# Kernel tuning notes

Hardware: AMD Instinct MI355X
Metric: run time of the kernel (lower is better)

The kernel has to match this reference:

```python
import jax, jax.numpy as jnp
import numpy as np
import math

D_MODEL = 768
N_HEADS = 12
HEAD_DIM = D_MODEL // N_HEADS
B, T = 2, 4096


def setup_inputs() -> dict:
    key = jax.random.key(0)
    k1, k2, k3, k4 = jax.random.split(key, 4)
    x = jax.random.normal(k1, (B, T, D_MODEL), dtype=jnp.float32)
    mask = jax.random.randint(k2, (B, T), 0, 2).astype(jnp.bool_)
    # torch Linear init scale ~ 1/sqrt(fan_in); use scaled normal for stability
    w_qkv = jax.random.normal(k3, (3 * D_MODEL, D_MODEL), dtype=jnp.float32) / math.sqrt(D_MODEL)
    w_proj = jax.random.normal(k4, (D_MODEL, D_MODEL), dtype=jnp.float32) / math.sqrt(D_MODEL)
    b_proj = jnp.zeros((D_MODEL,), dtype=jnp.float32)
    return {"x": x, "mask": mask, "w_qkv": w_qkv, "w_proj": w_proj, "b_proj": b_proj}


def reference(x, mask, w_qkv, w_proj, b_proj):
    Bb, Tt, D = x.shape
    H, Hd = N_HEADS, HEAD_DIM
    scale = math.sqrt(Hd)
    # qkv projection (bias-free): (B,T,3D) -> (3,B,H,T,Hd)
    qkv = jnp.einsum('btd,ed->bte', x, w_qkv)
    qkv = qkv.reshape(Bb, Tt, 3, H, Hd).transpose(2, 0, 3, 1, 4)
    q, k, v = qkv[0], qkv[1], qkv[2]
    # full T x T scores (faithful to non-fused original)
    attn = jnp.einsum('bhqd,bhkd->bhqk', q, k) / scale
    attn = jnp.where(mask[:, None, None, :], -jnp.inf, attn)
    attn = jax.nn.softmax(attn, axis=-1)  # dropout p=0 -> identity
    out = jnp.einsum('bhqk,bhkd->bhqd', attn, v)
    out = out.transpose(0, 2, 1, 3).reshape(Bb, Tt, D)
    return jnp.einsum('btd,ed->bte', out, w_proj) + b_proj
```

## Files before the change

kernel.cpp:

```cpp
#include <hip/hip_runtime.h>

#define D_MODEL 768
#define N_HEADS 12
#define SEQ 4096
#define KVB 64

typedef __attribute__((ext_vector_type(4))) float f32x4;
typedef __attribute__((ext_vector_type(16))) float f32x16;
typedef __attribute__((ext_vector_type(8))) short bf16x8;
typedef __attribute__((ext_vector_type(4))) unsigned short u16x4;

typedef __attribute__((address_space(3))) void lds_void;
typedef __attribute__((address_space(1))) const void glb_void;

static __device__ __forceinline__ void gld_lds16(const void* g, void* l) {
    __builtin_amdgcn_global_load_lds((glb_void*)g, (lds_void*)l, 16, 0, 0);
}

static __device__ __forceinline__ unsigned short f32_bf16(float f) {
    union { float f; unsigned int u; } c; c.f = f;
    unsigned int u = c.u;
    u += 0x7FFFu + ((u >> 16) & 1u);
    return (unsigned short)(u >> 16);
}

static __device__ __forceinline__ unsigned int cvtpk(float lo, float hi) {
    unsigned int r;
    asm("v_cvt_pk_bf16_f32 %0, %1, %2" : "=v"(r) : "v"(lo), "v"(hi));
    return r;
}

__global__ void cvt_bf16(const float* __restrict__ in, unsigned short* __restrict__ out, int n) {
    int i = (blockIdx.x * blockDim.x + threadIdx.x) * 4;
    int stride = gridDim.x * blockDim.x * 4;
    for (; i < n; i += stride) {
        f32x4 v = *(const f32x4*)(in + i);
        u16x4 o;
        o[0] = f32_bf16(v[0]); o[1] = f32_bf16(v[1]);
        o[2] = f32_bf16(v[2]); o[3] = f32_bf16(v[3]);
        *(u16x4*)(out + i) = o;
    }
}

#define QSCL 0.18033688f

__global__ __launch_bounds__(256) void qkv_gemm(const unsigned short* __restrict__ A,
                                                const unsigned short* __restrict__ Bw,
                                                unsigned short* __restrict__ qb,
                                                unsigned short* __restrict__ kb,
                                                unsigned short* __restrict__ vb) {
    __shared__ __attribute__((aligned(16))) unsigned short lA[128*32];
    __shared__ __attribute__((aligned(16))) unsigned short lB[128*32];
    const int K = 768;
    int tid = threadIdx.x;
    int wave = tid >> 6, lane = tid & 63;
    int qr = (wave >> 1) * 64, qc = (wave & 1) * 64;
    int m0 = blockIdx.x * 128, n0 = blockIdx.y * 128;
    f32x4 acc[4][4] = {};
    const int sl = (((lane >> 4) ^ (lane & 3)) * 16);

    for (int kt = 0; kt < K; kt += 32) {
        __syncthreads();
        #pragma unroll
        for (int i = 0; i < 2; ++i) {
            int c = i*256 + tid;
            int row = c >> 2;
            int col = ((c & 3) ^ (row & 3)) * 8;
            char* dA = (char*)lA + (i*256 + wave*64)*16;
            char* dB = (char*)lB + (i*256 + wave*64)*16;
            gld_lds16(A  + (size_t)(m0 + row) * K + kt + col, dA);
            gld_lds16(Bw + (size_t)(n0 + row) * K + kt + col, dB);
        }
        __syncthreads();
        bf16x8 af[4], bfr[4];
        #pragma unroll
        for (int m = 0; m < 4; ++m)
            af[m] = *(bf16x8*)((char*)lA + (qr + m*16 + (lane & 15))*64 + sl);
        #pragma unroll
        for (int n = 0; n < 4; ++n)
            bfr[n] = *(bf16x8*)((char*)lB + (qc + n*16 + (lane & 15))*64 + sl);
        #pragma unroll
        for (int m = 0; m < 4; ++m)
            #pragma unroll
            for (int n = 0; n < 4; ++n)
                acc[m][n] = __builtin_amdgcn_mfma_f32_16x16x32_bf16(af[m], bfr[n], acc[m][n], 0, 0, 0);
    }
    #pragma unroll
    for (int n = 0; n < 4; ++n) {
        int colg = n0 + qc + n*16 + (lane & 15);
        int s = colg / 768;
        int rem = colg - s * 768;
        int h = rem >> 6, d = rem & 63;
        if (s == 2) {
            #pragma unroll
            for (int m = 0; m < 4; ++m) {
                int rowb = m0 + qr + m*16 + (lane >> 4)*4;
                int bb = rowb >> 12, t0 = rowb & 4095;
                int t0p = (t0 & ~12) | ((t0 & 4) << 1) | ((t0 & 8) >> 1);
                u16x4 pk;
                #pragma unroll
                for (int r = 0; r < 4; ++r) pk[r] = f32_bf16(acc[m][n][r]);
                *(u16x4*)(vb + ((size_t)((bb*12 + h)*64 + d))*4096 + t0p) = pk;
            }
        } else {
            unsigned short* dst = (s == 0) ? qb : kb;
            float scl = (s == 0) ? QSCL : 1.0f;
            #pragma unroll
            for (int m = 0; m < 4; ++m) {
                int rowb = m0 + qr + m*16 + (lane >> 4)*4;
                #pragma unroll
                for (int r = 0; r < 4; ++r) {
                    int row = rowb + r;
                    int bb = row >> 12, t = row & 4095;
                    dst[((size_t)((bb*12 + h)*4096 + t))*64 + d] = f32_bf16(acc[m][n][r] * scl);
                }
            }
        }
    }
}

__global__ __launch_bounds__(512, 4) void attn_kern(const unsigned short* __restrict__ qbuf,
                                                    const unsigned short* __restrict__ kbuf,
                                                    const unsigned short* __restrict__ vtbuf,
                                                    const int* __restrict__ mask,
                                                    unsigned short* __restrict__ ob) {
    __shared__ __attribute__((aligned(16))) char lds[2][16384];
    __shared__ float lds_l[4][32];

    const int tid = threadIdx.x, wave = tid >> 6, lane = tid & 63;
    const int l31 = lane & 31, hi2 = lane >> 5;
    const int lane16 = lane * 16;
    const int wq = wave & 3, wk = wave >> 2;

    int raw = blockIdx.x;
    int sb = (raw & 7) * 96 + (raw >> 3);
    int bh = sb >> 5, qi = sb & 31;
    int q0 = qi * 128;
    int b = bh / 12, h = bh - b*12;

    const unsigned short* Qb = qbuf + (size_t)bh * SEQ * 64;
    const unsigned short* Kb = kbuf + (size_t)bh * SEQ * 64;
    const unsigned short* Vt = vtbuf + (size_t)bh * 64 * SEQ;
    const int* mrow = mask + b * SEQ;

    bf16x8 bq[4];
    #pragma unroll
    for (int ds = 0; ds < 4; ++ds)
        bq[ds] = *(const bf16x8*)(Qb + (size_t)(q0 + wq*32 + l31)*64 + ds*16 + hi2*8);

    union U4 { unsigned int w[4]; bf16x8 v; };
    U4 bext; bext.w[0] = (hi2 == 0) ? 0x3F80u : 0u; bext.w[1] = bext.w[2] = bext.w[3] = 0u;

    auto stage = [&](char* buf, int kv0) {
        #pragma unroll
        for (int i = 0; i < 2; ++i) {
            int fi = wave*2 + i;
            const unsigned short* gsrc;
            if (fi < 8) {
                int kt = fi >> 2, ds = fi & 3;
                gsrc = Kb + (size_t)(kv0 + kt*32 + l31)*64 + ds*16 + hi2*8;
            } else {
                int g = fi - 8, dt = g >> 2, ks = g & 3;
                gsrc = Vt + (size_t)(dt*32 + l31)*4096 + kv0 + ks*16 + hi2*8;
            }
            gld_lds16(gsrc, buf + fi*1024);
        }
    };

    f32x16 oacc0 = {}, oacc1 = {};
    float lr = 0.0f;

    stage(lds[0], 0);
    int mb = mrow[wk*32 + l31];
    __syncthreads();

    const int NT = SEQ / KVB;
    for (int t = 0; t < NT; ++t) {
        int kv0 = t * KVB;
        char* bufK = lds[t & 1];
        char* bufV = bufK + 8192;
        int mbn = 0;
        if (t + 1 < NT) {
            stage(lds[(t + 1) & 1], kv0 + KVB);
            mbn = mrow[kv0 + KVB + wk*32 + l31];
        }

        U4 ab;
        ab.w[0] = (hi2 == 0) ? (mb ? 0xC480u : 0xC18Au) : 0u;
        ab.w[1] = ab.w[2] = ab.w[3] = 0u;

        f32x16 s = {};
        s = __builtin_amdgcn_mfma_f32_32x32x16_bf16(ab.v, bext.v, s, 0, 0, 0);
        #pragma unroll
        for (int ds = 0; ds < 4; ++ds) {
            bf16x8 aK = *(bf16x8*)(bufK + (wk*4 + ds)*1024 + lane16);
            s = __builtin_amdgcn_mfma_f32_32x32x16_bf16(aK, bq[ds], s, 0, 0, 0);
        }

        float rs = 0.0f;
        #pragma unroll
        for (int i = 0; i < 16; ++i) { s[i] = __builtin_amdgcn_exp2f(s[i]); rs += s[i]; }
        rs += __shfl_xor(rs, 32);
        lr += rs;

        bf16x8 pa[2];
        #pragma unroll
        for (int ks = 0; ks < 2; ++ks) {
            U4 w;
            w.w[0] = cvtpk(s[8*ks+0], s[8*ks+1]);
            w.w[1] = cvtpk(s[8*ks+2], s[8*ks+3]);
            w.w[2] = cvtpk(s[8*ks+4], s[8*ks+5]);
            w.w[3] = cvtpk(s[8*ks+6], s[8*ks+7]);
            pa[ks] = w.v;
        }

        #pragma unroll
        for (int sb2 = 0; sb2 < 2; ++sb2) {
            int ksg = wk*2 + sb2;
            bf16x8 bv0 = *(bf16x8*)(bufV + (0*4 + ksg)*1024 + lane16);
            bf16x8 bv1 = *(bf16x8*)(bufV + (1*4 + ksg)*1024 + lane16);
            oacc0 = __builtin_amdgcn_mfma_f32_32x32x16_bf16(pa[sb2], bv0, oacc0, 0, 0, 0);
            oacc1 = __builtin_amdgcn_mfma_f32_32x32x16_bf16(pa[sb2], bv1, oacc1, 0, 0, 0);
        }

        __syncthreads();
        mb = mbn;
    }

    float* cbase = (float*)lds + wq * 2048;
    if (wk == 1) {
        #pragma unroll
        for (int i = 0; i < 16; ++i) {
            cbase[i*64 + lane]        = oacc0[i];
            cbase[(16 + i)*64 + lane] = oacc1[i];
        }
        if (lane < 32) lds_l[wq][lane] = lr;
    }
    __syncthreads();
    if (wk == 0 && lane < 32) lds_l[wq][lane] += lr;
    __syncthreads();
    if (wk == 0) {
        #pragma unroll
        for (int r = 0; r < 16; ++r) {
            int q = (r & 3) + 8*(r >> 2) + 4*hi2;
            float inv = 1.0f / lds_l[wq][q];
            int tg = q0 + wq*32 + q;
            size_t base = ((size_t)(b*SEQ + tg)) * D_MODEL + h*64 + l31;
            ob[base]      = f32_bf16((oacc0[r] + cbase[r*64 + lane])        * inv);
            ob[base + 32] = f32_bf16((oacc1[r] + cbase[(16 + r)*64 + lane]) * inv);
        }
    }
}

__global__ __launch_bounds__(256) void proj_gemm(const unsigned short* __restrict__ A,
                                                 const unsigned short* __restrict__ Bw,
                                                 const float* __restrict__ bias,
                                                 float* __restrict__ out) {
    __shared__ __attribute__((aligned(16))) unsigned short lA[128*32];
    __shared__ __attribute__((aligned(16))) unsigned short lB[128*32];
    const int K = 768;
    int tid = threadIdx.x;
    int wave = tid >> 6, lane = tid & 63;
    int qr = (wave >> 1) * 64, qc = (wave & 1) * 64;
    int m0 = blockIdx.x * 128, n0 = blockIdx.y * 128;
    f32x4 acc[4][4] = {};
    const int sl = (((lane >> 4) ^ (lane & 3)) * 16);

    for (int kt = 0; kt < K; kt += 32) {
        __syncthreads();
        #pragma unroll
        for (int i = 0; i < 2; ++i) {
            int c = i*256 + tid;
            int row = c >> 2;
            int col = ((c & 3) ^ (row & 3)) * 8;
            char* dA = (char*)lA + (i*256 + wave*64)*16;
            char* dB = (char*)lB + (i*256 + wave*64)*16;
            gld_lds16(A  + (size_t)(m0 + row) * K + kt + col, dA);
            gld_lds16(Bw + (size_t)(n0 + row) * K + kt + col, dB);
        }
        __syncthreads();
        bf16x8 af[4], bfr[4];
        #pragma unroll
        for (int m = 0; m < 4; ++m)
            af[m] = *(bf16x8*)((char*)lA + (qr + m*16 + (lane & 15))*64 + sl);
        #pragma unroll
        for (int n = 0; n < 4; ++n)
            bfr[n] = *(bf16x8*)((char*)lB + (qc + n*16 + (lane & 15))*64 + sl);
        #pragma unroll
        for (int m = 0; m < 4; ++m)
            #pragma unroll
            for (int n = 0; n < 4; ++n)
                acc[m][n] = __builtin_amdgcn_mfma_f32_16x16x32_bf16(af[m], bfr[n], acc[m][n], 0, 0, 0);
    }
    #pragma unroll
    for (int n = 0; n < 4; ++n) {
        int colg = n0 + qc + n*16 + (lane & 15);
        float bn = bias[colg];
        #pragma unroll
        for (int m = 0; m < 4; ++m) {
            int rowb = m0 + qr + m*16 + (lane >> 4)*4;
            #pragma unroll
            for (int r = 0; r < 4; ++r)
                out[(size_t)(rowb + r) * 768 + colg] = acc[m][n][r] + bn;
        }
    }
}

extern "C" void kernel_launch(void* const* d_in, const int* in_sizes, int n_in,
                              void* d_out, int out_size, void* d_ws, size_t ws_size,
                              hipStream_t stream) {
    const float* x      = (const float*)d_in[0];
    const int*   mask   = (const int*)d_in[1];
    const float* w_qkv  = (const float*)d_in[2];
    const float* w_proj = (const float*)d_in[3];
    const float* b_proj = (const float*)d_in[4];
    float* out = (float*)d_out;

    unsigned short* ws = (unsigned short*)d_ws;
    unsigned short* xb     = ws;
    unsigned short* wqkvb  = xb     + 6291456;
    unsigned short* wprojb = wqkvb  + 1769472;
    unsigned short* qb     = wprojb + 589824;
    unsigned short* kb     = qb     + 6291456;
    unsigned short* vtb    = kb     + 6291456;
    unsigned short* ob     = vtb    + 6291456;

    cvt_bf16<<<1024, 256, 0, stream>>>(x,      xb,     6291456);
    cvt_bf16<<<256,  256, 0, stream>>>(w_qkv,  wqkvb,  1769472);
    cvt_bf16<<<128,  256, 0, stream>>>(w_proj, wprojb, 589824);

    qkv_gemm<<<dim3(64, 18), 256, 0, stream>>>(xb, wqkvb, qb, kb, vtb);
    attn_kern<<<768, 512, 0, stream>>>(qb, kb, vtb, mask, ob);
    proj_gemm<<<dim3(64, 6), 256, 0, stream>>>(ob, wprojb, b_proj, out);
}
```

Before: 235.8 us.

## Triple-buffer K/V tiles in attention with partial vmcnt waits

Replaces the double-buffered LDS staging in the attention loop with a three-stage ring, prefetching two KV tiles ahead. The full __syncthreads is replaced by an explicit s_waitcnt vmcnt(3) plus s_barrier, so each iteration waits only for the oldest tile's global-to-LDS loads and the next prefetch stays in flight. This aims to hide global load latency better. In exchange LDS use grows from 32KB to 48KB per block, which may lower occupancy under launch_bounds(512,4). The hand-written vmcnt counts also depend on the exact number of outstanding loads per iteration.

```diff
diff --git a/kernel.cpp b/kernel.cpp
--- a/kernel.cpp
+++ b/kernel.cpp
@@ -124,7 +124,7 @@
                                                     const unsigned short* __restrict__ vtbuf,
                                                     const int* __restrict__ mask,
                                                     unsigned short* __restrict__ ob) {
-    __shared__ __attribute__((aligned(16))) char lds[2][16384];
+    __shared__ __attribute__((aligned(16))) char lds[3][16384];
     __shared__ float lds_l[4][32];
 
     const int tid = threadIdx.x, wave = tid >> 6, lane = tid & 63;
@@ -141,12 +141,13 @@
     const unsigned short* Qb = qbuf + (size_t)bh * SEQ * 64;
     const unsigned short* Kb = kbuf + (size_t)bh * SEQ * 64;
     const unsigned short* Vt = vtbuf + (size_t)bh * 64 * SEQ;
-    const int* mrow = mask + b * SEQ;
+    const int* mrow = mask + b * SEQ + wk*32 + l31;
 
     bf16x8 bq[4];
     #pragma unroll
     for (int ds = 0; ds < 4; ++ds)
         bq[ds] = *(const bf16x8*)(Qb + (size_t)(q0 + wq*32 + l31)*64 + ds*16 + hi2*8);
+    __builtin_amdgcn_sched_barrier(0);
 
     union U4 { unsigned int w[4]; bf16x8 v; };
     U4 bext; bext.w[0] = (hi2 == 0) ? 0x3F80u : 0u; bext.w[1] = bext.w[2] = bext.w[3] = 0u;
@@ -170,23 +171,31 @@
     f32x16 oacc0 = {}, oacc1 = {};
     float lr = 0.0f;
 
-    stage(lds[0], 0);
-    int mb = mrow[wk*32 + l31];
-    __syncthreads();
+    char* bA = lds[0];
+    char* bB = lds[1];
+    char* bC = lds[2];
+
+    stage(bA, 0);
+    int mb0 = mrow[0];
+    stage(bB, KVB);
+    int mb1 = mrow[KVB];
+    asm volatile("s_waitcnt vmcnt(3)" ::: "memory");
+    __builtin_amdgcn_sched_barrier(0);
+    __builtin_amdgcn_s_barrier();
+    __builtin_amdgcn_sched_barrier(0);
 
     const int NT = SEQ / KVB;
     for (int t = 0; t < NT; ++t) {
-        int kv0 = t * KVB;
-        char* bufK = lds[t & 1];
-        char* bufV = bufK + 8192;
-        int mbn = 0;
-        if (t + 1 < NT) {
-            stage(lds[(t + 1) & 1], kv0 + KVB);
-            mbn = mrow[kv0 + KVB + wk*32 + l31];
-        }
+        int mb2 = 0;
+        if (t + 2 < NT) {
+            stage(bC, (t + 2) * KVB);
+            mb2 = mrow[(t + 2) * KVB];
+        }
+        char* bufK = bA;
+        char* bufV = bA + 8192;
 
         U4 ab;
-        ab.w[0] = (hi2 == 0) ? (mb ? 0xC480u : 0xC18Au) : 0u;
+        ab.w[0] = (hi2 == 0) ? (mb0 ? 0xC480u : 0xC18Au) : 0u;
         ab.w[1] = ab.w[2] = ab.w[3] = 0u;
 
         f32x16 s = {};
@@ -223,8 +232,17 @@
             oacc1 = __builtin_amdgcn_mfma_f32_32x32x16_bf16(pa[sb2], bv1, oacc1, 0, 0, 0);
         }
 
-        __syncthreads();
-        mb = mbn;
+        if (t + 2 < NT) {
+            asm volatile("s_waitcnt vmcnt(3)" ::: "memory");
+        } else {
+            asm volatile("s_waitcnt vmcnt(0)" ::: "memory");
+        }
+        __builtin_amdgcn_sched_barrier(0);
+        __builtin_amdgcn_s_barrier();
+        __builtin_amdgcn_sched_barrier(0);
+
+        char* tmp = bA; bA = bB; bB = bC; bC = tmp;
+        mb0 = mb1; mb1 = mb2;
     }
 
     float* cbase = (float*)lds + wq * 2048;
```

Result: no change. 239.3 us (+1.5%).
